# Kernel optimization log

Hardware: AMD Instinct MI355X
Metric: run time of the kernel (lower is better)

The kernel has to match this reference:

```python
import jax, jax.numpy as jnp
import numpy as np


def setup_inputs() -> dict:
    key = jax.random.key(0)
    ks = jax.random.split(key, 7)
    B, T, inp_d, hid_d = 16, 4095, 2048, 2048
    scale = 0.02
    return {
        "x": jax.random.normal(ks[0], (B, inp_d), dtype=jnp.float32),
        "K_his": jax.random.normal(ks[1], (B, T, hid_d), dtype=jnp.float32),
        "V_his": jax.random.normal(ks[2], (B, T, hid_d), dtype=jnp.float32),
        "W_attn": jax.random.normal(ks[3], (inp_d, 3 * hid_d), dtype=jnp.float32) * scale,
        "b_attn": jax.random.normal(ks[4], (3 * hid_d,), dtype=jnp.float32) * scale,
        "W_proj": jax.random.normal(ks[5], (hid_d, hid_d), dtype=jnp.float32) * scale,
        "b_proj": jax.random.normal(ks[6], (hid_d,), dtype=jnp.float32) * scale,
        "n_head": 16,
    }


def reference(x, K_his, V_his, W_attn, b_attn, W_proj, b_proj, n_head):
    B = x.shape[0]
    qkv = x @ W_attn + b_attn                      # [B, 3*hid_d]
    q, k, v = jnp.split(qkv, 3, axis=-1)           # each [B, hid_d]
    hid_d = q.shape[-1]
    dh = hid_d // n_head
    # append current step to the KV cache
    K = jnp.concatenate([K_his, k[:, None, :]], axis=1)  # [B, T, hid_d]
    V = jnp.concatenate([V_his, v[:, None, :]], axis=1)
    T = K.shape[1]
    Kh = K.reshape(B, T, n_head, dh).transpose(0, 2, 1, 3)  # [B, H, T, dh]
    Vh = V.reshape(B, T, n_head, dh).transpose(0, 2, 1, 3)  # [B, H, T, dh]
    qh = q.reshape(B, n_head, dh, 1)                        # [B, H, dh, 1]
    scores = Kh @ qh                                        # [B, H, T, 1]
    # NOTE: faithful to the source: softmax over dim=-1 which has size 1 -> all ones
    att = jax.nn.softmax(scores, axis=-1)                   # [B, H, T, 1]
    v_next = jnp.swapaxes(Vh, -1, -2) @ att                 # [B, H, dh, 1]
    v_next = v_next.reshape(B, hid_d) @ W_proj + b_proj     # [B, hid_d]
    # faithful: reshape the head-major layout back to [B, T, hid_d]
    K_out = Kh.reshape(B, -1, hid_d)
    V_out = Vh.reshape(B, -1, hid_d)
    return K_out, V_out, v_next
```

## Files before the change

kernel.cpp:

```cpp
#include <hip/hip_runtime.h>


typedef float f4 __attribute__((ext_vector_type(4)));

__global__ void init_kernel(const float* __restrict__ b_attn,
                            const float* __restrict__ b_proj,
                            float* __restrict__ qkv,
                            float* __restrict__ colsum,
                            float* __restrict__ vnext) {
  int tid = blockIdx.x * blockDim.x + threadIdx.x;
  qkv[tid] = b_attn[2048 + (tid & 4095)];
  if (tid < 32768) {
    colsum[tid] = 0.0f;
    vnext[tid] = b_proj[tid & 2047];
  }
}

__global__ void small_gemm_atomic(const float* __restrict__ X,
                                  const float* __restrict__ W,
                                  int ldw, int col0,
                                  float* __restrict__ out, int ncols) {
  int j  = blockIdx.x * 512 + threadIdx.x * 2;
  int k0 = blockIdx.y * 64;
  const float* wp = W + (size_t)k0 * ldw + col0 + j;
  float2 acc[16];
#pragma unroll
  for (int b = 0; b < 16; ++b) acc[b] = make_float2(0.f, 0.f);
  for (int kk = 0; kk < 64; ++kk) {
    float2 w = *(const float2*)(wp + (size_t)kk * ldw);
    const float* xp = X + k0 + kk;
#pragma unroll
    for (int b = 0; b < 16; ++b) {
      float xv = xp[(size_t)b * 2048];
      acc[b].x = fmaf(xv, w.x, acc[b].x);
      acc[b].y = fmaf(xv, w.y, acc[b].y);
    }
  }
#pragma unroll
  for (int b = 0; b < 16; ++b) {
    atomicAdd(&out[b * ncols + j],     acc[b].x);
    atomicAdd(&out[b * ncols + j + 1], acc[b].y);
  }
}

__global__ void __launch_bounds__(256, 2)
copy_transpose(const float* __restrict__ K_his,
               const float* __restrict__ V_his,
               const float* __restrict__ qkv,
               float* __restrict__ out,
               float* __restrict__ colsum) {
  const int b     = blockIdx.y;
  const int which = blockIdx.z;
  const int gx    = blockIdx.x;
  const int tid   = threadIdx.x;
  const int l     = tid & 63;
  const int w     = tid >> 6;
  const int off   = 4 * (l & 31);
  const bool hi   = (l >= 32);

  const float* src  = which ? V_his : K_his;
  const float* srcb = src + (size_t)b * 8386560ull;
  const float* qsrc = qkv + b * 4096 + which * 2048;
  float* outb = out + ((size_t)which << 27) + ((size_t)b << 23);

  __shared__ float lds[8192];

  f4 accA[8], accB[8];
#pragma unroll
  for (int i = 0; i < 8; ++i) {
    accA[i] = (f4){0.f, 0.f, 0.f, 0.f};
    accB[i] = (f4){0.f, 0.f, 0.f, 0.f};
  }

  for (int gsub = 0; gsub < 2; ++gsub) {
    const int g = gx * 2 + gsub;
#pragma unroll
    for (int it = 0; it < 2; ++it) {
      const int rp = it * 4 + w;
      const int t0 = g * 16 + rp * 2;
      const float* r0 = srcb + (size_t)t0 * 2048u;
      const float* r1 = (t0 + 1 == 4095) ? qsrc : (r0 + 2048);
      const float* rowp = hi ? r1 : r0;

      f4 sa[8], sb[8];
#pragma unroll
      for (int i = 0; i < 8; ++i) {
        sa[i] = __builtin_nontemporal_load((const f4*)(rowp + i * 256 + off));
        sb[i] = __builtin_nontemporal_load((const f4*)(rowp + i * 256 + 128 + off));
      }
      if (which) {
#pragma unroll
        for (int i = 0; i < 8; ++i) { accA[i] += sa[i]; accB[i] += sb[i]; }
      }
#pragma unroll
      for (int i = 0; i < 8; ++i) {
        float* o0 = outb + (size_t)(2 * i * 256 + g) * 2048u + (unsigned)(rp * 256 + 4 * l);
        __builtin_nontemporal_store(sa[i], (f4*)o0);
        __builtin_nontemporal_store(sb[i], (f4*)(o0 + 256 * 2048));
      }
    }
  }

  if (which) {
#pragma unroll
    for (int i = 0; i < 8; ++i) {
      accA[i].x += __shfl_xor(accA[i].x, 32);
      accA[i].y += __shfl_xor(accA[i].y, 32);
      accA[i].z += __shfl_xor(accA[i].z, 32);
      accA[i].w += __shfl_xor(accA[i].w, 32);
      accB[i].x += __shfl_xor(accB[i].x, 32);
      accB[i].y += __shfl_xor(accB[i].y, 32);
      accB[i].z += __shfl_xor(accB[i].z, 32);
      accB[i].w += __shfl_xor(accB[i].w, 32);
    }
    if (l < 32) {
#pragma unroll
      for (int i = 0; i < 8; ++i) {
        *(f4*)(&lds[w * 2048 + i * 256 + off])       = accA[i];
        *(f4*)(&lds[w * 2048 + i * 256 + 128 + off]) = accB[i];
      }
    }
    __syncthreads();
    const int c = tid * 8;
    f4 s0 = *(const f4*)(&lds[c]) + *(const f4*)(&lds[2048 + c])
          + *(const f4*)(&lds[4096 + c]) + *(const f4*)(&lds[6144 + c]);
    f4 s1 = *(const f4*)(&lds[c + 4]) + *(const f4*)(&lds[2048 + c + 4])
          + *(const f4*)(&lds[4096 + c + 4]) + *(const f4*)(&lds[6144 + c + 4]);
    float* cp = colsum + b * 2048 + c;
    atomicAdd(cp + 0, s0.x); atomicAdd(cp + 1, s0.y);
    atomicAdd(cp + 2, s0.z); atomicAdd(cp + 3, s0.w);
    atomicAdd(cp + 4, s1.x); atomicAdd(cp + 5, s1.y);
    atomicAdd(cp + 6, s1.z); atomicAdd(cp + 7, s1.w);
  }
}

extern "C" void kernel_launch(void* const* d_in, const int* in_sizes, int n_in,
                              void* d_out, int out_size, void* d_ws, size_t ws_size,
                              hipStream_t stream) {
  const float* x      = (const float*)d_in[0];
  const float* K_his  = (const float*)d_in[1];
  const float* V_his  = (const float*)d_in[2];
  const float* W_attn = (const float*)d_in[3];
  const float* b_attn = (const float*)d_in[4];
  const float* W_proj = (const float*)d_in[5];
  const float* b_proj = (const float*)d_in[6];

  float* out    = (float*)d_out;
  float* qkv    = (float*)d_ws;
  float* colsum = qkv + 16 * 4096;
  float* vnext  = out + 268435456ull;

  init_kernel<<<256, 256, 0, stream>>>(b_attn, b_proj, qkv, colsum, vnext);
  small_gemm_atomic<<<dim3(8, 32), 256, 0, stream>>>(x, W_attn, 6144, 2048, qkv, 4096);
  copy_transpose<<<dim3(128, 16, 2), 256, 0, stream>>>(K_his, V_his, qkv, out, colsum);
  small_gemm_atomic<<<dim3(4, 32), 256, 0, stream>>>(colsum, W_proj, 2048, 0, vnext, 2048);
}
```

Measured before the change: 488.8 us.

## Load contiguous rows per wavefront and cross-lane shuffle into transposed stores

Each wavefront now reads a full 256-float contiguous chunk of each of two rows instead of splitting lanes across the two rows. It then uses cross-half shuffles to form the interleaved output vectors. Column-sum accumulation now adds both rows per lane directly, which removes the shuffle-reduction before the LDS stage. Each block also handles four row groups instead of two, so half as many blocks launch, and the occupancy hint goes from 2 to 3 blocks per CU. The added per-element shuffles and the register pressure from the higher occupancy target could offset the gain from better load coalescing.

```diff
diff --git a/kernel.cpp b/kernel.cpp
--- a/kernel.cpp
+++ b/kernel.cpp
@@ -43,7 +43,7 @@
   }
 }
 
-__global__ void __launch_bounds__(256, 2)
+__global__ void __launch_bounds__(256, 3)
 copy_transpose(const float* __restrict__ K_his,
                const float* __restrict__ V_his,
                const float* __restrict__ qkv,
@@ -51,75 +51,66 @@
                float* __restrict__ colsum) {
   const int b     = blockIdx.y;
   const int which = blockIdx.z;
-  const int gx    = blockIdx.x;
+  const int gblk  = blockIdx.x;
   const int tid   = threadIdx.x;
   const int l     = tid & 63;
   const int w     = tid >> 6;
-  const int off   = 4 * (l & 31);
   const bool hi   = (l >= 32);
 
   const float* src  = which ? V_his : K_his;
-  const float* srcb = src + (size_t)b * 8386560ull;
-  const float* qsrc = qkv + b * 4096 + which * 2048;
+  const float* srcb = src + (size_t)b * 8386560ull + (unsigned)(4 * l);
+  const float* qsrc = qkv + b * 4096 + which * 2048 + 4 * l;
   float* outb = out + ((size_t)which << 27) + ((size_t)b << 23);
 
   __shared__ float lds[8192];
 
-  f4 accA[8], accB[8];
+  f4 acc[8];
 #pragma unroll
-  for (int i = 0; i < 8; ++i) {
-    accA[i] = (f4){0.f, 0.f, 0.f, 0.f};
-    accB[i] = (f4){0.f, 0.f, 0.f, 0.f};
-  }
+  for (int i = 0; i < 8; ++i) acc[i] = (f4){0.f, 0.f, 0.f, 0.f};
 
-  for (int gsub = 0; gsub < 2; ++gsub) {
-    const int g = gx * 2 + gsub;
+  for (int gs = 0; gs < 4; ++gs) {
+    const int g = gblk * 4 + gs;
 #pragma unroll
-    for (int it = 0; it < 2; ++it) {
-      const int rp = it * 4 + w;
+    for (int rpi = 0; rpi < 2; ++rpi) {
+      const int rp = rpi * 4 + w;
       const int t0 = g * 16 + rp * 2;
       const float* r0 = srcb + (size_t)t0 * 2048u;
       const float* r1 = (t0 + 1 == 4095) ? qsrc : (r0 + 2048);
-      const float* rowp = hi ? r1 : r0;
 
-      f4 sa[8], sb[8];
+      f4 rA[8], rB[8];
+#pragma unroll
+      for (int i = 0; i < 8; ++i)
+        rA[i] = __builtin_nontemporal_load((const f4*)(r0 + i * 256));
+#pragma unroll
+      for (int i = 0; i < 8; ++i)
+        rB[i] = __builtin_nontemporal_load((const f4*)(r1 + i * 256));
+
+      if (which) {
+#pragma unroll
+        for (int i = 0; i < 8; ++i) acc[i] += rA[i] + rB[i];
+      }
+
 #pragma unroll
       for (int i = 0; i < 8; ++i) {
-        sa[i] = __builtin_nontemporal_load((const f4*)(rowp + i * 256 + off));
-        sb[i] = __builtin_nontemporal_load((const f4*)(rowp + i * 256 + 128 + off));
-      }
-      if (which) {
+        f4 H0, H1;
 #pragma unroll
-        for (int i = 0; i < 8; ++i) { accA[i] += sa[i]; accB[i] += sb[i]; }
-      }
-#pragma unroll
-      for (int i = 0; i < 8; ++i) {
+        for (int c = 0; c < 4; ++c) {
+          float ax = __shfl_xor(rA[i][c], 32);
+          float bx = __shfl_xor(rB[i][c], 32);
+          H0[c] = hi ? bx : rA[i][c];
+          H1[c] = hi ? rB[i][c] : ax;
+        }
         float* o0 = outb + (size_t)(2 * i * 256 + g) * 2048u + (unsigned)(rp * 256 + 4 * l);
-        __builtin_nontemporal_store(sa[i], (f4*)o0);
-        __builtin_nontemporal_store(sb[i], (f4*)(o0 + 256 * 2048));
+        __builtin_nontemporal_store(H0, (f4*)o0);
+        __builtin_nontemporal_store(H1, (f4*)(o0 + 256 * 2048));
       }
     }
   }
 
   if (which) {
 #pragma unroll
-    for (int i = 0; i < 8; ++i) {
-      accA[i].x += __shfl_xor(accA[i].x, 32);
-      accA[i].y += __shfl_xor(accA[i].y, 32);
-      accA[i].z += __shfl_xor(accA[i].z, 32);
-      accA[i].w += __shfl_xor(accA[i].w, 32);
-      accB[i].x += __shfl_xor(accB[i].x, 32);
-      accB[i].y += __shfl_xor(accB[i].y, 32);
-      accB[i].z += __shfl_xor(accB[i].z, 32);
-      accB[i].w += __shfl_xor(accB[i].w, 32);
-    }
-    if (l < 32) {
-#pragma unroll
-      for (int i = 0; i < 8; ++i) {
-        *(f4*)(&lds[w * 2048 + i * 256 + off])       = accA[i];
-        *(f4*)(&lds[w * 2048 + i * 256 + 128 + off]) = accB[i];
-      }
-    }
+    for (int i = 0; i < 8; ++i)
+      *(f4*)(&lds[w * 2048 + i * 256 + 4 * l]) = acc[i];
     __syncthreads();
     const int c = tid * 8;
     f4 s0 = *(const f4*)(&lds[c]) + *(const f4*)(&lds[2048 + c])
@@ -152,6 +143,6 @@
 
   init_kernel<<<256, 256, 0, stream>>>(b_attn, b_proj, qkv, colsum, vnext);
   small_gemm_atomic<<<dim3(8, 32), 256, 0, stream>>>(x, W_attn, 6144, 2048, qkv, 4096);
-  copy_transpose<<<dim3(128, 16, 2), 256, 0, stream>>>(K_his, V_his, qkv, out, colsum);
+  copy_transpose<<<dim3(64, 16, 2), 256, 0, stream>>>(K_his, V_his, qkv, out, colsum);
   small_gemm_atomic<<<dim3(4, 32), 256, 0, stream>>>(colsum, W_proj, 2048, 0, vnext, 2048);
 }
```

Result: faster. 466.9 us (-4.5%).
